# Kernel tuning notes

Hardware: AMD Instinct MI355X
Metric: run time of the kernel (lower is better)

Reference implementation:

```python
import jax, jax.numpy as jnp
import numpy as np

N = 120000   # nodes
E = 1200000  # edges
F_IN = 14    # PascalVOC-SP node features
H = 64       # args.hidden
C = 21       # num_classes
EPS = 1e-5


def _glorot(k, shape):
    fan_in = shape[0]
    return jax.random.normal(k, shape, jnp.float32) / np.sqrt(fan_in).astype(np.float32)


def setup_inputs() -> dict:
    key = jax.random.key(0)
    ks = jax.random.split(key, 16)
    inp = {}
    inp['x1'] = jax.random.normal(ks[0], (N, F_IN), jnp.float32)
    inp['edge_index'] = jax.random.randint(ks[1], (2, E), 0, N)
    dims = [(F_IN, H), (H, H), (H, H), (H, H)]
    i = 2
    for l, (din, dout) in enumerate(dims, 1):
        inp[f'Wn{l}'] = _glorot(ks[i], (din, dout)); i += 1
        inp[f'Wr{l}'] = _glorot(ks[i], (din, dout)); i += 1
        inp[f'b{l}'] = jnp.zeros((dout,), jnp.float32)
    for l in (1, 2, 3):
        inp[f'g{l}'] = jnp.ones((H,), jnp.float32)
        inp[f'be{l}'] = jnp.zeros((H,), jnp.float32)
    inp['Wm0'] = _glorot(ks[10], (H, H))
    inp['gm0'] = jnp.ones((H,), jnp.float32)
    inp['bem0'] = jnp.zeros((H,), jnp.float32)
    inp['Wm1'] = _glorot(ks[11], (H, H))
    inp['gm1'] = jnp.ones((H,), jnp.float32)
    inp['bem1'] = jnp.zeros((H,), jnp.float32)
    inp['Wm2'] = _glorot(ks[12], (H, C))
    inp['bm2'] = jnp.zeros((C,), jnp.float32)
    return inp


def _bn(x, g, b):
    # BatchNorm1d forward with batch statistics (train-mode normalization, biased var)
    m = x.mean(axis=0)
    v = x.var(axis=0)
    return (x - m) * jax.lax.rsqrt(v + EPS) * g + b


def _sage(x, src, dst, Wn, Wr, b):
    # PyG SAGEConv (mean aggr): out = mean_neighbors @ Wn + b + x @ Wr
    s = jax.ops.segment_sum(x[src], dst, num_segments=N)        # [N, d]
    cnt = jax.ops.segment_sum(jnp.ones((src.shape[0],), x.dtype), dst, num_segments=N)
    mean = s / jnp.maximum(cnt, 1.0)[:, None]
    return mean @ Wn + b + x @ Wr


def _lrelu(z):
    return jnp.where(z > 0, z, 0.01 * z)


def reference(x1, edge_index, Wn1, Wr1, b1, Wn2, Wr2, b2, Wn3, Wr3, b3, Wn4, Wr4, b4,
              g1, be1, g2, be2, g3, be3, Wm0, gm0, bem0, Wm1, gm1, bem1, Wm2, bm2):
    src, dst = edge_index[0], edge_index[1]
    x = _bn(_lrelu(_sage(x1, src, dst, Wn1, Wr1, b1)), g1, be1)   # conv1 + bano1 (dropout off)
    x = _bn(_lrelu(_sage(x, src, dst, Wn2, Wr2, b2)), g2, be2)    # conv2 + bano2
    x = _bn(jax.nn.relu(_sage(x, src, dst, Wn3, Wr3, b3)), g3, be3)  # conv3 + bano3
    x = _sage(x, src, dst, Wn4, Wr4, b4)                          # conv4
    # mlpRep: Linear(no bias)->BN->ReLU x2, then Linear(bias), no final act
    x = jax.nn.relu(_bn(x @ Wm0, gm0, bem0))
    x = jax.nn.relu(_bn(x @ Wm1, gm1, bem1))
    return x @ Wm2 + bm2
```

## Files before the change

### kernel.cpp

```cpp
#include <hip/hip_runtime.h>

constexpr int NN = 120000;
constexpr int EE = 1200000;
constexpr float EPSV = 1e-5f;
constexpr int NMFMABLK = NN / 64;
constexpr int ASTRIDE = 32;
constexpr int NSLOT = 64;

constexpr int BNODES  = 128;
constexpr int NBUCK   = (NN + BNODES - 1) / BNODES;
constexpr int BSTRIDE = 1536;
constexpr int EPB3    = 4096;
constexpr int NB3     = (EE + EPB3 - 1) / EPB3;
constexpr int NSTATF  = 5*NSLOT*128;

typedef __attribute__((ext_vector_type(8))) short bf8v;
typedef __attribute__((ext_vector_type(4))) float f4v;

__device__ __forceinline__ float bf2f(unsigned short u){
  union { unsigned i; float f; } v; v.i = ((unsigned)u) << 16; return v.f;
}
__device__ __forceinline__ unsigned short f2bf(float f){
  union { float f; unsigned i; } v; v.f = f;
  unsigned u = v.i;
  return (unsigned short)((u + 0x7FFFu + ((u >> 16) & 1u)) >> 16);
}
__device__ __forceinline__ unsigned pack2(float a, float b){
  return (unsigned)f2bf(a) | ((unsigned)f2bf(b) << 16);
}
__device__ __forceinline__ float act_f(float z, int ACT){
  if (ACT == 1) return z > 0.0f ? z : 0.01f*z;
  if (ACT == 2) return fmaxf(z, 0.0f);
  return z;
}
__device__ __forceinline__ void acc8(uint4 u, float& a0, float& a1, float& a2, float& a3,
                                     float& a4, float& a5, float& a6, float& a7){
  a0 += bf2f((unsigned short)(u.x & 0xFFFF)); a1 += bf2f((unsigned short)(u.x >> 16));
  a2 += bf2f((unsigned short)(u.y & 0xFFFF)); a3 += bf2f((unsigned short)(u.y >> 16));
  a4 += bf2f((unsigned short)(u.z & 0xFFFF)); a5 += bf2f((unsigned short)(u.z >> 16));
  a6 += bf2f((unsigned short)(u.w & 0xFFFF)); a7 += bf2f((unsigned short)(u.w >> 16));
}

__global__ __launch_bounds__(512) void k_bucket(const int* __restrict__ src, const int* __restrict__ dst,
                                                int* __restrict__ cursor, unsigned* __restrict__ bucketed,
                                                float* __restrict__ stats,
                                                const float* __restrict__ x, unsigned* __restrict__ xb){
  __shared__ int hist[NBUCK];
  __shared__ int lstart[NBUCK];
  const int tid = threadIdx.x;
  const int e0  = blockIdx.x * EPB3;
  for (int i = blockIdx.x*512 + tid; i < NSTATF; i += NB3*512) stats[i] = 0.0f;
  for (int i = blockIdx.x*512 + tid; i < NN*8; i += NB3*512){
    int n = i >> 3, j = i & 7;
    int c0 = 2*j, c1 = 2*j + 1;
    float f0 = (c0 < 14) ? x[(size_t)n*14 + c0] : 0.0f;
    float f1 = (c1 < 14) ? x[(size_t)n*14 + c1] : 0.0f;
    xb[i] = pack2(f0, f1);
  }
  for (int i = tid; i < NBUCK; i += 512) hist[i] = 0;
  __syncthreads();

  const bool full = (e0 + EPB3 <= EE);
  if (full){
    #pragma unroll 4
    for (int k = 0; k < EPB3/512; k++){
      int d = dst[e0 + k*512 + tid];
      atomicAdd(&hist[d >> 7], 1);
    }
  } else {
    #pragma unroll 1
    for (int k = 0; k < EPB3/512; k++){
      int e = e0 + k*512 + tid;
      if (e < EE){
        int d = dst[e];
        atomicAdd(&hist[d >> 7], 1);
      }
    }
  }
  __syncthreads();
  for (int i = tid; i < NBUCK; i += 512){
    int h = hist[i];
    lstart[i] = (h > 0) ? atomicAdd(&cursor[i], h) : 0;
  }
  __syncthreads();
  for (int i = tid; i < NBUCK; i += 512) hist[i] = 0;
  __syncthreads();
  #pragma unroll 1
  for (int k = 0; k < EPB3/512; k++){
    int e = e0 + k*512 + tid;
    if (e < EE){
      int d = dst[e];
      int s = src[e];
      int b = d >> 7;
      int r = atomicAdd(&hist[b], 1);
      int idx = lstart[b] + r;
      if (idx < BSTRIDE)
        bucketed[(size_t)b*BSTRIDE + idx] = ((unsigned)s << 7) | (unsigned)(d & 127);
    }
  }
}

__global__ __launch_bounds__(256) void k_buildadj(const unsigned* __restrict__ bucketed,
                                                  const int* __restrict__ cursor,
                                                  int* __restrict__ cnt, int* __restrict__ adj,
                                                  float* __restrict__ invdeg){
  __shared__ alignas(16) int ladj[BNODES*ASTRIDE];
  __shared__ int lcnt[BNODES];
  const int tid = threadIdx.x;
  const int b   = blockIdx.x;
  if (tid < BNODES) lcnt[tid] = 0;
  __syncthreads();
  const int tot = min(cursor[b], BSTRIDE);
  const unsigned* rp = bucketed + (size_t)b*BSTRIDE;
  for (int e = tid; e < tot; e += 256){
    unsigned rec = rp[e];
    int d = (int)(rec & 127u);
    int s = (int)(rec >> 7);
    int p = atomicAdd(&lcnt[d], 1);
    if (p < ASTRIDE) ladj[d*ASTRIDE + p] = s;
  }
  __syncthreads();
  int4* ap = (int4*)(adj + (size_t)b*BNODES*ASTRIDE);
  const int4* lp = (const int4*)ladj;
  #pragma unroll
  for (int i = 0; i < (BNODES*ASTRIDE/4)/256; i++)
    ap[i*256 + tid] = lp[i*256 + tid];
  if (tid < BNODES){
    int c = lcnt[tid];
    int n = b*BNODES + tid;
    cnt[n] = c;
    invdeg[n] = (c > 0) ? (1.0f/(float)c) : -1.0f;
  }
}

__global__ __launch_bounds__(256) void k_prep_conv_frag(const float* __restrict__ Wn, const float* __restrict__ Wr,
                                                        const float* __restrict__ b, const float* __restrict__ statSlots,
                                                        const float* __restrict__ g, const float* __restrict__ be,
                                                        unsigned short* __restrict__ frag, float* __restrict__ bias2){
  __shared__ float sc[64], sh[64];
  int t = threadIdx.x;
  if (t < 64){
    float sum = 0.0f, sq = 0.0f;
    #pragma unroll 8
    for (int s = 0; s < NSLOT; s++){
      sum += statSlots[s*128 + t];
      sq  += statSlots[s*128 + 64 + t];
    }
    float m = sum * (1.0f/NN);
    float v = sq * (1.0f/NN) - m*m;
    float a = g[t] * rsqrtf(v + EPSV);
    sc[t] = a; sh[t] = be[t] - m*a;
  }
  __syncthreads();
  if (blockIdx.x == 0 && t < 64){
    float accB = b[t], accN = 0.0f;
    for (int k=0;k<64;k++){
      accB += sh[k]*Wr[k*64+t];
      accN += sh[k]*Wn[k*64+t];
    }
    bias2[t]      = accB;
    bias2[64 + t] = accN;
  }
  {
    int idx = blockIdx.x*256 + t;
    int j    = idx & 7;
    int lane = (idx >> 3) & 63;
    int kk   = (idx >> 9) & 1;
    int ct   = (idx >> 10) & 3;
    int mat  = (idx >> 12) & 1;
    int k    = kk*32 + (lane >> 4)*8 + j;
    int col  = ct*16 + (lane & 15);
    const float* W = mat ? Wr : Wn;
    frag[idx] = f2bf(sc[k] * W[k*64 + col]);
  }
}

__global__ __launch_bounds__(256) void k_prep_lin_frag(const float* __restrict__ W,
                                                       unsigned short* __restrict__ frag,
                                                       float* __restrict__ bias2,
                                                       const float* __restrict__ bnSlots,
                                                       float* __restrict__ bnRed){
  int t = threadIdx.x;
  if (blockIdx.x == 0 && t < 128){
    bias2[t] = 0.0f;
    if (bnSlots){
      float s = 0.0f;
      #pragma unroll 8
      for (int sl = 0; sl < NSLOT; sl++) s += bnSlots[sl*128 + t];
      bnRed[t] = s;
    }
  }
  {
    int idx = blockIdx.x*256 + t;
    int j    = idx & 7;
    int lane = (idx >> 3) & 63;
    int kk   = (idx >> 9) & 1;
    int ct   = (idx >> 10) & 3;
    int k    = kk*32 + (lane >> 4)*8 + j;
    int col  = ct*16 + (lane & 15);
    frag[idx] = f2bf(W[k*64 + col]);
  }
}

__global__ __launch_bounds__(256) void k_prep_c1_frag(const float* __restrict__ Wn, const float* __restrict__ Wr,
                                                      const float* __restrict__ b,
                                                      unsigned short* __restrict__ frag, float* __restrict__ bias2){
  int t = threadIdx.x;
  int idx = blockIdx.x*256 + t;
  int j    = idx & 7;
  int lane = (idx >> 3) & 63;
  int ct   = (idx >> 9) & 3;
  int k    = (lane >> 4)*8 + j;
  int col  = ct*16 + (lane & 15);
  float w = 0.0f;
  if (k < 14)                 w = Wn[k*64 + col];
  else if (k >= 16 && k < 30) w = Wr[(k-16)*64 + col];
  frag[idx] = f2bf(w);
  if (blockIdx.x == 0 && t < 64) bias2[t] = b[t];
}

__global__ __launch_bounds__(64) void k_prep_aff(const float* __restrict__ st,
                                                 const float* __restrict__ g, const float* __restrict__ be,
                                                 float* __restrict__ aff){
  int t = threadIdx.x;
  float s = 0.0f, q = 0.0f;
  #pragma unroll 8
  for (int sl = 0; sl < NSLOT; sl++){
    s += st[sl*128 + t];
    q += st[sl*128 + 64 + t];
  }
  float m = s*(1.0f/NN);
  float v = q*(1.0f/NN) - m*m;
  float a = g[t]*rsqrtf(v+EPSV);
  aff[t]      = a;
  aff[64 + t] = be[t] - m*a;
}

template<int ACT, bool STATS>
__global__ __launch_bounds__(256, 1) void k_gmfma(const unsigned short* __restrict__ X,
                                                  const int* __restrict__ cnt, const int* __restrict__ adj,
                                                  const float* __restrict__ invdeg,
                                                  const unsigned short* __restrict__ frag,
                                                  const float* __restrict__ bias2,
                                                  unsigned short* __restrict__ out,
                                                  float* __restrict__ statsOut){
  __shared__ unsigned short sMean[64*72];
  __shared__ float sst[512];
  const int tid  = threadIdx.x;
  const int lane = tid & 63;
  const int wv   = tid >> 6;
  const int nb0  = blockIdx.x*64;

  {
    const int q8 = lane & 7;
    const int h8 = lane >> 3;
    #pragma unroll
    for (int t8 = 0; t8 < 2; t8++){
      const int row = wv*16 + h8*2 + t8;
      const int n   = nb0 + row;
      const int d   = min(cnt[n], ASTRIDE);
      const int st  = n*ASTRIDE;
      float a0=0,a1=0,a2=0,a3=0,a4=0,a5=0,a6=0,a7=0;
      int j = 0;
      for (; j + 7 < d; j += 8){
        int4 sa = *(const int4*)(adj + st + j);
        int4 sb = *(const int4*)(adj + st + j + 4);
        uint4 u0 = *(const uint4*)(X + (size_t)sa.x*64 + 8*q8);
        uint4 u1 = *(const uint4*)(X + (size_t)sa.y*64 + 8*q8);
        uint4 u2 = *(const uint4*)(X + (size_t)sa.z*64 + 8*q8);
        uint4 u3 = *(const uint4*)(X + (size_t)sa.w*64 + 8*q8);
        uint4 u4 = *(const uint4*)(X + (size_t)sb.x*64 + 8*q8);
        uint4 u5 = *(const uint4*)(X + (size_t)sb.y*64 + 8*q8);
        uint4 u6 = *(const uint4*)(X + (size_t)sb.z*64 + 8*q8);
        uint4 u7 = *(const uint4*)(X + (size_t)sb.w*64 + 8*q8);
        acc8(u0,a0,a1,a2,a3,a4,a5,a6,a7); acc8(u1,a0,a1,a2,a3,a4,a5,a6,a7);
        acc8(u2,a0,a1,a2,a3,a4,a5,a6,a7); acc8(u3,a0,a1,a2,a3,a4,a5,a6,a7);
        acc8(u4,a0,a1,a2,a3,a4,a5,a6,a7); acc8(u5,a0,a1,a2,a3,a4,a5,a6,a7);
        acc8(u6,a0,a1,a2,a3,a4,a5,a6,a7); acc8(u7,a0,a1,a2,a3,a4,a5,a6,a7);
      }
      for (; j + 3 < d; j += 4){
        int4 sa = *(const int4*)(adj + st + j);
        uint4 u0 = *(const uint4*)(X + (size_t)sa.x*64 + 8*q8);
        uint4 u1 = *(const uint4*)(X + (size_t)sa.y*64 + 8*q8);
        uint4 u2 = *(const uint4*)(X + (size_t)sa.z*64 + 8*q8);
        uint4 u3 = *(const uint4*)(X + (size_t)sa.w*64 + 8*q8);
        acc8(u0,a0,a1,a2,a3,a4,a5,a6,a7); acc8(u1,a0,a1,a2,a3,a4,a5,a6,a7);
        acc8(u2,a0,a1,a2,a3,a4,a5,a6,a7); acc8(u3,a0,a1,a2,a3,a4,a5,a6,a7);
      }
      for (; j < d; j++){
        int s = adj[st + j];
        uint4 u = *(const uint4*)(X + (size_t)s*64 + 8*q8);
        acc8(u,a0,a1,a2,a3,a4,a5,a6,a7);
      }
      float iv = fmaxf(invdeg[n], 0.0f);
      uint4 o;
      o.x = pack2(a0*iv, a1*iv);
      o.y = pack2(a2*iv, a3*iv);
      o.z = pack2(a4*iv, a5*iv);
      o.w = pack2(a6*iv, a7*iv);
      *(uint4*)(sMean + row*72 + 8*q8) = o;
    }
  }

  const bf8v* fp = (const bf8v*)frag;
  bf8v wn[4][2], wr[4][2];
  #pragma unroll
  for (int ct=0;ct<4;ct++){
    #pragma unroll
    for (int kk=0;kk<2;kk++){
      wn[ct][kk] = fp[((0*4+ct)*2+kk)*64 + lane];
      wr[ct][kk] = fp[((1*4+ct)*2+kk)*64 + lane];
    }
  }
  const int m  = lane & 15;
  const int kq = lane >> 4;
  const size_t arow = (size_t)(nb0 + wv*16 + m)*64;
  bf8v ax0 = *(const bf8v*)(X + arow + kq*8);
  bf8v ax1 = *(const bf8v*)(X + arow + 32 + kq*8);
  __syncthreads();
  bf8v am0 = *(const bf8v*)(sMean + (wv*16 + m)*72 + kq*8);
  bf8v am1 = *(const bf8v*)(sMean + (wv*16 + m)*72 + 32 + kq*8);

  f4v acc[4];
  #pragma unroll
  for (int ct=0;ct<4;ct++){
    f4v c = {0.0f,0.0f,0.0f,0.0f};
    c = __builtin_amdgcn_mfma_f32_16x16x32_bf16(am0, wn[ct][0], c, 0,0,0);
    c = __builtin_amdgcn_mfma_f32_16x16x32_bf16(am1, wn[ct][1], c, 0,0,0);
    c = __builtin_amdgcn_mfma_f32_16x16x32_bf16(ax0, wr[ct][0], c, 0,0,0);
    c = __builtin_amdgcn_mfma_f32_16x16x32_bf16(ax1, wr[ct][1], c, 0,0,0);
    acc[ct] = c;
  }

  const int col = lane & 15;
  float bb[4], bg[4];
  #pragma unroll
  for (int ct=0;ct<4;ct++){
    bb[ct] = bias2[ct*16 + col];
    bg[ct] = bias2[64 + ct*16 + col];
  }
  float ls[4] = {0,0,0,0}, lq[4] = {0,0,0,0};
  #pragma unroll
  for (int r=0;r<4;r++){
    const int node = nb0 + wv*16 + (lane>>4)*4 + r;
    float gadd = (invdeg[node] > 0.0f) ? 1.0f : 0.0f;
    #pragma unroll
    for (int ct=0;ct<4;ct++){
      float z = acc[ct][r] + bb[ct] + gadd * bg[ct];
      z = act_f(z, ACT);
      out[(size_t)node*64 + ct*16 + col] = f2bf(z);
      if (STATS){ ls[ct] += z; lq[ct] = fmaf(z, z, lq[ct]); }
    }
  }
  if constexpr (STATS){
    #pragma unroll
    for (int ct=0;ct<4;ct++){
      float s = ls[ct]; s += __shfl_down(s, 32); s += __shfl_down(s, 16);
      float q = lq[ct]; q += __shfl_down(q, 32); q += __shfl_down(q, 16);
      if (kq == 0){
        sst[wv*128 + ct*16 + col]      = s;
        sst[wv*128 + 64 + ct*16 + col] = q;
      }
    }
    __syncthreads();
    if (tid < 128){
      float v = sst[tid] + sst[128+tid] + sst[256+tid] + sst[384+tid];
      atomicAdd(&statsOut[(blockIdx.x & (NSLOT-1))*128 + tid], v);
    }
  }
}

template<int ACT, bool STATS, bool BNA>
__global__ __launch_bounds__(256, 1) void k_mfma_lin(const unsigned short* __restrict__ Ax,
                                                     const unsigned short* __restrict__ frag,
                                                     const float* __restrict__ bias2,
                                                     unsigned short* __restrict__ out,
                                                     float* __restrict__ statsOut,
                                                     const float* __restrict__ bnRed,
                                                     const float* __restrict__ bnG,
                                                     const float* __restrict__ bnB){
  __shared__ float sst[512];
  const int lane = threadIdx.x & 63;
  const int wv   = threadIdx.x >> 6;
  const int n0   = (blockIdx.x*4 + wv)*16;
  const int m    = lane & 15;
  const int kq   = lane >> 4;

  const bf8v* fp = (const bf8v*)frag;
  bf8v wr[4][2];
  #pragma unroll
  for (int ct=0;ct<4;ct++){
    #pragma unroll
    for (int kk=0;kk<2;kk++) wr[ct][kk] = fp[(ct*2+kk)*64 + lane];
  }

  const size_t arow = (size_t)(n0 + m)*64;
  bf8v ax0 = *(const bf8v*)(Ax + arow + kq*8);
  bf8v ax1 = *(const bf8v*)(Ax + arow + 32 + kq*8);
  if constexpr (BNA){
    #pragma unroll
    for (int j=0;j<8;j++){
      int k0 = kq*8 + j, k1 = 32 + kq*8 + j;
      float m0 = bnRed[k0]*(1.0f/NN);
      float v0 = bnRed[64+k0]*(1.0f/NN) - m0*m0;
      float a0 = bnG[k0]*rsqrtf(v0+EPSV);
      float b0 = bnB[k0] - m0*a0;
      ax0[j] = (short)f2bf(fmaxf(fmaf(a0, bf2f((unsigned short)ax0[j]), b0), 0.0f));
      float m1 = bnRed[k1]*(1.0f/NN);
      float v1 = bnRed[64+k1]*(1.0f/NN) - m1*m1;
      float a1 = bnG[k1]*rsqrtf(v1+EPSV);
      float b1 = bnB[k1] - m1*a1;
      ax1[j] = (short)f2bf(fmaxf(fmaf(a1, bf2f((unsigned short)ax1[j]), b1), 0.0f));
    }
  }

  f4v acc[4];
  #pragma unroll
  for (int ct=0;ct<4;ct++){
    f4v c = {0.0f,0.0f,0.0f,0.0f};
    c = __builtin_amdgcn_mfma_f32_16x16x32_bf16(ax0, wr[ct][0], c, 0,0,0);
    c = __builtin_amdgcn_mfma_f32_16x16x32_bf16(ax1, wr[ct][1], c, 0,0,0);
    acc[ct] = c;
  }

  const int col = lane & 15;
  float bb[4];
  #pragma unroll
  for (int ct=0;ct<4;ct++) bb[ct] = bias2[ct*16 + col];
  float ls[4] = {0,0,0,0}, lq[4] = {0,0,0,0};
  #pragma unroll
  for (int r=0;r<4;r++){
    const int node = n0 + (lane>>4)*4 + r;
    #pragma unroll
    for (int ct=0;ct<4;ct++){
      float z = act_f(acc[ct][r] + bb[ct], ACT);
      out[(size_t)node*64 + ct*16 + col] = f2bf(z);
      if (STATS){ ls[ct] += z; lq[ct] = fmaf(z, z, lq[ct]); }
    }
  }
  if constexpr (STATS){
    #pragma unroll
    for (int ct=0;ct<4;ct++){
      float s = ls[ct]; s += __shfl_down(s, 32); s += __shfl_down(s, 16);
      float q = lq[ct]; q += __shfl_down(q, 32); q += __shfl_down(q, 16);
      if (kq == 0){
        sst[wv*128 + ct*16 + col]      = s;
        sst[wv*128 + 64 + ct*16 + col] = q;
      }
    }
    __syncthreads();
    if (threadIdx.x < 128){
      float v = sst[threadIdx.x] + sst[128+threadIdx.x] + sst[256+threadIdx.x] + sst[384+threadIdx.x];
      atomicAdd(&statsOut[(blockIdx.x & (NSLOT-1))*128 + threadIdx.x], v);
    }
  }
}

__global__ __launch_bounds__(256, 1) void k_conv1m(const unsigned* __restrict__ xb,
                                                   const int* __restrict__ cnt, const int* __restrict__ adj,
                                                   const float* __restrict__ invdeg,
                                                   const unsigned short* __restrict__ frag,
                                                   const float* __restrict__ bias2,
                                                   unsigned short* __restrict__ out,
                                                   float* __restrict__ statsOut){
  __shared__ unsigned short sMean[64*24];
  __shared__ float sst[512];
  const int tid  = threadIdx.x;
  const int lane = tid & 63;
  const int wv   = tid >> 6;
  const int nb0  = blockIdx.x*64;

  {
    const int q2 = lane & 1;
    const int g  = (lane >> 1) & 1;
    const int nd = lane >> 2;
    const int row = wv*16 + nd;
    const int n   = nb0 + row;
    const int d   = min(cnt[n], ASTRIDE);
    const int st  = n*ASTRIDE;
    float a0=0,a1=0,a2=0,a3=0,a4=0,a5=0,a6=0,a7=0;
    int j = g;
    for (; j + 2 < d; j += 4){
      int s0 = adj[st + j];
      int s1 = adj[st + j + 2];
      uint4 u0 = *(const uint4*)(xb + s0*8 + q2*4);
      uint4 u1 = *(const uint4*)(xb + s1*8 + q2*4);
      acc8(u0,a0,a1,a2,a3,a4,a5,a6,a7);
      acc8(u1,a0,a1,a2,a3,a4,a5,a6,a7);
    }
    if (j < d){
      int s0 = adj[st + j];
      uint4 u0 = *(const uint4*)(xb + s0*8 + q2*4);
      acc8(u0,a0,a1,a2,a3,a4,a5,a6,a7);
    }
    a0 += __shfl_xor(a0, 2); a1 += __shfl_xor(a1, 2);
    a2 += __shfl_xor(a2, 2); a3 += __shfl_xor(a3, 2);
    a4 += __shfl_xor(a4, 2); a5 += __shfl_xor(a5, 2);
    a6 += __shfl_xor(a6, 2); a7 += __shfl_xor(a7, 2);
    if (g == 0){
      float iv = fmaxf(invdeg[n], 0.0f);
      uint4 o;
      o.x = pack2(a0*iv, a1*iv);
      o.y = pack2(a2*iv, a3*iv);
      o.z = pack2(a4*iv, a5*iv);
      o.w = pack2(a6*iv, a7*iv);
      *(uint4*)(sMean + row*24 + q2*8) = o;
    }
  }

  const bf8v* fp = (const bf8v*)frag;
  bf8v wb[4];
  #pragma unroll
  for (int ct=0;ct<4;ct++) wb[ct] = fp[ct*64 + lane];

  const int m  = lane & 15;
  const int kq = lane >> 4;
  __syncthreads();
  bf8v av;
  if (kq < 2){
    av = *(const bf8v*)(sMean + (wv*16 + m)*24 + kq*8);
  } else {
    const unsigned short* xr = (const unsigned short*)xb + (size_t)(nb0 + wv*16 + m)*16;
    av = *(const bf8v*)(xr + (kq-2)*8);
  }

  f4v acc[4];
  #pragma unroll
  for (int ct=0;ct<4;ct++){
    f4v c = {0.0f,0.0f,0.0f,0.0f};
    c = __builtin_amdgcn_mfma_f32_16x16x32_bf16(av, wb[ct], c, 0,0,0);
    acc[ct] = c;
  }

  const int col = lane & 15;
  float bb[4];
  #pragma unroll
  for (int ct=0;ct<4;ct++) bb[ct] = bias2[ct*16 + col];
  float ls[4] = {0,0,0,0}, lq[4] = {0,0,0,0};
  #pragma unroll
  for (int r=0;r<4;r++){
    const int node = nb0 + wv*16 + (lane>>4)*4 + r;
    #pragma unroll
    for (int ct=0;ct<4;ct++){
      float z = act_f(acc[ct][r] + bb[ct], 1);
      out[(size_t)node*64 + ct*16 + col] = f2bf(z);
      ls[ct] += z; lq[ct] = fmaf(z, z, lq[ct]);
    }
  }
  #pragma unroll
  for (int ct=0;ct<4;ct++){
    float s = ls[ct]; s += __shfl_down(s, 32); s += __shfl_down(s, 16);
    float q = lq[ct]; q += __shfl_down(q, 32); q += __shfl_down(q, 16);
    if (kq == 0){
      sst[wv*128 + ct*16 + col]      = s;
      sst[wv*128 + 64 + ct*16 + col] = q;
    }
  }
  __syncthreads();
  if (tid < 128){
    float v = sst[tid] + sst[128+tid] + sst[256+tid] + sst[384+tid];
    atomicAdd(&statsOut[(blockIdx.x & (NSLOT-1))*128 + tid], v);
  }
}

__global__ __launch_bounds__(256, 1) void k_lin21(const unsigned short* __restrict__ x,
                                                  const float* __restrict__ W, const float* __restrict__ bias,
                                                  const float* __restrict__ aff,
                                                  float* __restrict__ out){
  __shared__ float sW[64*21];
  __shared__ float sAff[128];
  const int tid = threadIdx.x;
  if (tid < 128) sAff[tid] = aff[tid];
  for (int i = tid; i < 64*21; i += 256) sW[i] = W[i];
  __syncthreads();

  const int p  = tid & 3;
  const int nl = tid >> 2;
  const int n  = blockIdx.x*64 + nl;
  const bool valid = (n < NN);
  const int k0 = p*16;

  uint4 u0 = {0,0,0,0}, u1 = {0,0,0,0};
  if (valid){
    const unsigned short* rp = x + (size_t)n*64 + k0;
    u0 = *(const uint4*)(rp);
    u1 = *(const uint4*)(rp + 8);
  }
  float f[16];
  f[0]=bf2f((unsigned short)(u0.x&0xFFFF)); f[1]=bf2f((unsigned short)(u0.x>>16));
  f[2]=bf2f((unsigned short)(u0.y&0xFFFF)); f[3]=bf2f((unsigned short)(u0.y>>16));
  f[4]=bf2f((unsigned short)(u0.z&0xFFFF)); f[5]=bf2f((unsigned short)(u0.z>>16));
  f[6]=bf2f((unsigned short)(u0.w&0xFFFF)); f[7]=bf2f((unsigned short)(u0.w>>16));
  f[8]=bf2f((unsigned short)(u1.x&0xFFFF)); f[9]=bf2f((unsigned short)(u1.x>>16));
  f[10]=bf2f((unsigned short)(u1.y&0xFFFF)); f[11]=bf2f((unsigned short)(u1.y>>16));
  f[12]=bf2f((unsigned short)(u1.z&0xFFFF)); f[13]=bf2f((unsigned short)(u1.z>>16));
  f[14]=bf2f((unsigned short)(u1.w&0xFFFF)); f[15]=bf2f((unsigned short)(u1.w>>16));
  #pragma unroll
  for (int j=0;j<16;j++)
    f[j] = fmaxf(fmaf(sAff[k0+j], f[j], sAff[64+k0+j]), 0.0f);

  float a[21];
  #pragma unroll
  for (int jj=0;jj<21;jj++) a[jj] = 0.0f;
  #pragma unroll
  for (int k=0;k<16;k++){
    const float* wr = sW + (k0+k)*21;
    float rv = f[k];
    #pragma unroll
    for (int jj=0;jj<21;jj++) a[jj] = fmaf(wr[jj], rv, a[jj]);
  }
  #pragma unroll
  for (int jj=0;jj<21;jj++){
    a[jj] += __shfl_xor(a[jj], 1);
    a[jj] += __shfl_xor(a[jj], 2);
  }
  if (valid){
    const int c0 = p*6;
    const int ce = (p == 3) ? 21 : c0 + 6;
    float* op = out + (size_t)n*21;
    #pragma unroll 6
    for (int jj=c0; jj<ce; jj++) op[jj] = a[jj] + bias[jj];
  }
}

extern "C" void kernel_launch(void* const* d_in, const int* in_sizes, int n_in,
                              void* d_out, int out_size, void* d_ws, size_t ws_size,
                              hipStream_t stream){
  const float* x1  = (const float*)d_in[0];
  const int*   ei  = (const int*)d_in[1];
  const int* srcp = ei;
  const int* dstp = ei + EE;
  const float *Wn1=(const float*)d_in[2],  *Wr1=(const float*)d_in[3],  *b1=(const float*)d_in[4];
  const float *Wn2=(const float*)d_in[5],  *Wr2=(const float*)d_in[6],  *b2=(const float*)d_in[7];
  const float *Wn3=(const float*)d_in[8],  *Wr3=(const float*)d_in[9],  *b3=(const float*)d_in[10];
  const float *Wn4=(const float*)d_in[11], *Wr4=(const float*)d_in[12], *b4=(const float*)d_in[13];
  const float *g1=(const float*)d_in[14], *be1=(const float*)d_in[15];
  const float *g2=(const float*)d_in[16], *be2=(const float*)d_in[17];
  const float *g3=(const float*)d_in[18], *be3=(const float*)d_in[19];
  const float *Wm0=(const float*)d_in[20], *gm0=(const float*)d_in[21], *bem0=(const float*)d_in[22];
  const float *Wm1=(const float*)d_in[23], *gm1=(const float*)d_in[24], *bem1=(const float*)d_in[25];
  const float *Wm2=(const float*)d_in[26], *bm2=(const float*)d_in[27];
  float* out = (float*)d_out;

  char* ws = (char*)d_ws;
  int*   cnt     = (int*)(ws);
  float* invdeg  = (float*)(ws + (1ull<<20));
  int*   adj     = (int*)(ws + (2ull<<20));
  unsigned short* hA   = (unsigned short*)(ws + (25ull<<20));
  unsigned short* hB   = (unsigned short*)(ws + (41ull<<20));
  float* stats   = (float*)(ws + (57ull<<20));
  float* bnRed   = (float*)(ws + (57ull<<20) + 192*1024);
  float* aff5    = (float*)(ws + (57ull<<20) + 224*1024);
  unsigned short* fragC = (unsigned short*)(ws + (58ull<<20));
  float* bias2C  = (float*)(ws + (58ull<<20) + 65536);
  unsigned short* fragL = (unsigned short*)(ws + (59ull<<20));
  float* bias2L  = (float*)(ws + (59ull<<20) + 65536);
  unsigned* xb   = (unsigned*)(ws + (60ull<<20));
  unsigned short* frag1 = (unsigned short*)(ws + (64ull<<20));
  float* bias1   = (float*)(ws + (64ull<<20) + 8192);
  unsigned* bucketed = (unsigned*)(ws + (25ull<<20));
  int* cursor        = (int*)(ws + (25ull<<20) + (6ull<<20));

  float* S1 = stats;
  float* S2 = stats + NSLOT*128;
  float* S3 = stats + 2*NSLOT*128;
  float* S4 = stats + 3*NSLOT*128;
  float* S5 = stats + 4*NSLOT*128;

  hipMemsetAsync(cursor, 0, NBUCK*sizeof(int), stream);
  k_bucket  <<<NB3,  512,0,stream>>>(srcp, dstp, cursor, bucketed, stats, x1, xb);
  k_buildadj<<<NBUCK,256,0,stream>>>(bucketed, cursor, cnt, adj, invdeg);

  k_prep_c1_frag<<<8,256,0,stream>>>(Wn1, Wr1, b1, frag1, bias1);
  k_conv1m<<<NMFMABLK,256,0,stream>>>(xb, cnt, adj, invdeg, frag1, bias1, hA, S1);

  k_prep_conv_frag<<<32,256,0,stream>>>(Wn2,Wr2,b2,S1,g1,be1,fragC,bias2C);
  k_gmfma<1,true><<<NMFMABLK,256,0,stream>>>(hA,cnt,adj,invdeg,fragC,bias2C,hB,S2);

  k_prep_conv_frag<<<32,256,0,stream>>>(Wn3,Wr3,b3,S2,g2,be2,fragC,bias2C);
  k_gmfma<2,true><<<NMFMABLK,256,0,stream>>>(hB,cnt,adj,invdeg,fragC,bias2C,hA,S3);

  k_prep_conv_frag<<<32,256,0,stream>>>(Wn4,Wr4,b4,S3,g3,be3,fragC,bias2C);
  k_gmfma<0,false><<<NMFMABLK,256,0,stream>>>(hA,cnt,adj,invdeg,fragC,bias2C,hB,nullptr);

  k_prep_lin_frag<<<16,256,0,stream>>>(Wm0, fragL, bias2L, nullptr, nullptr);
  k_mfma_lin<0,true,false><<<NMFMABLK,256,0,stream>>>(hB,fragL,bias2L,hA,S4,nullptr,nullptr,nullptr);

  k_prep_lin_frag<<<16,256,0,stream>>>(Wm1, fragL, bias2L, S4, bnRed);
  k_mfma_lin<0,true,true><<<NMFMABLK,256,0,stream>>>(hA,fragL,bias2L,hB,S5,bnRed,gm0,bem0);

  k_prep_aff<<<1,64,0,stream>>>(S5, gm1, bem1, aff5);
  k_lin21<<<NMFMABLK,256,0,stream>>>(hB,Wm2,bm2,aff5,out);
}
```

Measured before the change: 348.6 us.

## Stage adjacency lists in LDS and split neighbors across lane pairs in gather

The gather phase of the fused SAGE+MFMA kernel now copies each wave's 16 nodes' padded adjacency rows into shared memory with coalesced int4 loads. Each node is handled by 4 lanes: two split the neighbor list in interleaved pairs and two split the feature halves, looping over 4 feature chunks. Partial sums are combined with a shuffle before writing the bf16 mean to LDS. The aim is to raise memory-level parallelism and cut serialized per-lane index loads. The cost is more loop iterations over feature chunks, re-reading indices four times, and extra LDS use.

After: 462.1 us. +32.6%, slower.

```diff
diff --git a/kernel.cpp b/kernel.cpp
--- a/kernel.cpp
+++ b/kernel.cpp
@@ -245,6 +245,7 @@
                                                   unsigned short* __restrict__ out,
                                                   float* __restrict__ statsOut){
   __shared__ unsigned short sMean[64*72];
+  __shared__ int sAdj[4][16][34];
   __shared__ float sst[512];
   const int tid  = threadIdx.x;
   const int lane = tid & 63;
@@ -252,53 +253,61 @@
   const int nb0  = blockIdx.x*64;
 
   {
-    const int q8 = lane & 7;
-    const int h8 = lane >> 3;
-    #pragma unroll
-    for (int t8 = 0; t8 < 2; t8++){
-      const int row = wv*16 + h8*2 + t8;
-      const int n   = nb0 + row;
-      const int d   = min(cnt[n], ASTRIDE);
-      const int st  = n*ASTRIDE;
+    const int4* gp = (const int4*)(adj + (size_t)(nb0 + wv*16)*ASTRIDE);
+    #pragma unroll
+    for (int i = 0; i < 2; i++){
+      int idx = i*64 + lane;
+      int4 v = gp[idx];
+      int row = idx >> 3, ch = idx & 7;
+      sAdj[wv][row][ch*4+0] = v.x;
+      sAdj[wv][row][ch*4+1] = v.y;
+      sAdj[wv][row][ch*4+2] = v.z;
+      sAdj[wv][row][ch*4+3] = v.w;
+    }
+  }
+
+  {
+    const int nd = lane >> 2;
+    const int g  = (lane >> 1) & 1;
+    const int q  = lane & 1;
+    const int row = wv*16 + nd;
+    const int n   = nb0 + row;
+    const int d   = min(cnt[n], ASTRIDE);
+    const float iv = fmaxf(invdeg[n], 0.0f);
+    #pragma unroll
+    for (int t = 0; t < 4; t++){
+      const int foff = t*16 + q*8;
       float a0=0,a1=0,a2=0,a3=0,a4=0,a5=0,a6=0,a7=0;
-      int j = 0;
-      for (; j + 7 < d; j += 8){
-        int4 sa = *(const int4*)(adj + st + j);
-        int4 sb = *(const int4*)(adj + st + j + 4);
-        uint4 u0 = *(const uint4*)(X + (size_t)sa.x*64 + 8*q8);
-        uint4 u1 = *(const uint4*)(X + (size_t)sa.y*64 + 8*q8);
-        uint4 u2 = *(const uint4*)(X + (size_t)sa.z*64 + 8*q8);
-        uint4 u3 = *(const uint4*)(X + (size_t)sa.w*64 + 8*q8);
-        uint4 u4 = *(const uint4*)(X + (size_t)sb.x*64 + 8*q8);
-        uint4 u5 = *(const uint4*)(X + (size_t)sb.y*64 + 8*q8);
-        uint4 u6 = *(const uint4*)(X + (size_t)sb.z*64 + 8*q8);
-        uint4 u7 = *(const uint4*)(X + (size_t)sb.w*64 + 8*q8);
-        acc8(u0,a0,a1,a2,a3,a4,a5,a6,a7); acc8(u1,a0,a1,a2,a3,a4,a5,a6,a7);
-        acc8(u2,a0,a1,a2,a3,a4,a5,a6,a7); acc8(u3,a0,a1,a2,a3,a4,a5,a6,a7);
-        acc8(u4,a0,a1,a2,a3,a4,a5,a6,a7); acc8(u5,a0,a1,a2,a3,a4,a5,a6,a7);
-        acc8(u6,a0,a1,a2,a3,a4,a5,a6,a7); acc8(u7,a0,a1,a2,a3,a4,a5,a6,a7);
+      int m = 0;
+      for (; 4*m + 2*g + 1 < d; m++){
+        int j = 4*m + 2*g;
+        int s0 = sAdj[wv][nd][j];
+        int s1 = sAdj[wv][nd][j+1];
+        uint4 u0 = *(const uint4*)(X + (size_t)s0*64 + foff);
+        uint4 u1 = *(const uint4*)(X + (size_t)s1*64 + foff);
+        acc8(u0,a0,a1,a2,a3,a4,a5,a6,a7);
+        acc8(u1,a0,a1,a2,a3,a4,a5,a6,a7);
       }
-      for (; j + 3 < d; j += 4){
-        int4 sa = *(const int4*)(adj + st + j);
-        uint4 u0 = *(const uint4*)(X + (size_t)sa.x*64 + 8*q8);
-        uint4 u1 = *(const uint4*)(X + (size_t)sa.y*64 + 8*q8);
-        uint4 u2 = *(const uint4*)(X + (size_t)sa.z*64 + 8*q8);
-        uint4 u3 = *(const uint4*)(X + (size_t)sa.w*64 + 8*q8);
-        acc8(u0,a0,a1,a2,a3,a4,a5,a6,a7); acc8(u1,a0,a1,a2,a3,a4,a5,a6,a7);
-        acc8(u2,a0,a1,a2,a3,a4,a5,a6,a7); acc8(u3,a0,a1,a2,a3,a4,a5,a6,a7);
+      {
+        int j = 4*m + 2*g;
+        if (j < d){
+          int s0 = sAdj[wv][nd][j];
+          uint4 u0 = *(const uint4*)(X + (size_t)s0*64 + foff);
+          acc8(u0,a0,a1,a2,a3,a4,a5,a6,a7);
+        }
       }
-      for (; j < d; j++){
-        int s = adj[st + j];
-        uint4 u = *(const uint4*)(X + (size_t)s*64 + 8*q8);
-        acc8(u,a0,a1,a2,a3,a4,a5,a6,a7);
+      a0 += __shfl_xor(a0, 2); a1 += __shfl_xor(a1, 2);
+      a2 += __shfl_xor(a2, 2); a3 += __shfl_xor(a3, 2);
+      a4 += __shfl_xor(a4, 2); a5 += __shfl_xor(a5, 2);
+      a6 += __shfl_xor(a6, 2); a7 += __shfl_xor(a7, 2);
+      if (g == 0){
+        uint4 o;
+        o.x = pack2(a0*iv, a1*iv);
+        o.y = pack2(a2*iv, a3*iv);
+        o.z = pack2(a4*iv, a5*iv);
+        o.w = pack2(a6*iv, a7*iv);
+        *(uint4*)(sMean + row*72 + foff) = o;
       }
-      float iv = fmaxf(invdeg[n], 0.0f);
-      uint4 o;
-      o.x = pack2(a0*iv, a1*iv);
-      o.y = pack2(a2*iv, a3*iv);
-      o.z = pack2(a4*iv, a5*iv);
-      o.w = pack2(a6*iv, a7*iv);
-      *(uint4*)(sMean + row*72 + 8*q8) = o;
     }
   }
 
```
